# Performance work log

Hardware: AMD Instinct MI355X
Metric: run time of the kernel (lower is better)

Reference implementation:

```python
import jax, jax.numpy as jnp
import numpy as np

N, C, E, NUM_ID, NUM_LABELS = 50000, 128, 1600000, 2048, 7


def setup_inputs() -> dict:
    key = jax.random.key(0)
    k_x, k_r, k_c, k_id, k_lab, k_w, k_wid = jax.random.split(key, 7)
    x = jax.random.normal(k_x, (N, C), dtype=jnp.float32)
    row = jax.random.randint(k_r, (E,), 0, N)
    col = jax.random.randint(k_c, (E,), 0, N)
    # remove accidental self-loops so the 'add remaining self loops' step
    # (append all N self loops) matches PyG's add_remaining_self_loops exactly
    col = jnp.where(col == row, (col + 1) % N, col)
    edge_index = jnp.stack([row, col]).astype(jnp.int64)
    idx = jax.random.randint(k_id, (NUM_ID,), 0, N).astype(jnp.int64)
    node_label = jax.random.randint(k_lab, (N,), 0, 8).astype(jnp.int64)
    # glorot init
    s = jnp.sqrt(6.0 / (C + C)).astype(jnp.float32)
    weight = jax.random.uniform(k_w, (C, C), minval=-s, maxval=s, dtype=jnp.float32)
    weight_id = jax.random.uniform(k_wid, (NUM_LABELS, C, C), minval=-s, maxval=s, dtype=jnp.float32)
    return {"x": x, "edge_index": edge_index, "id": idx, "node_label": node_label,
            "weight": weight, "weight_id": weight_id}


def reference(x, edge_index, id, node_label, weight, weight_id):
    n = x.shape[0]
    row, col = edge_index[0], edge_index[1]
    # ego-center update: x[id] += x[id] @ W (index_add handles duplicate ids)
    x = x.at[id].add(x[id] @ weight)
    # label-grouped gather-matmul-scatter: ox = x + sum_i mask_i * (x @ W_i)
    ox = x
    for i in range(NUM_LABELS):
        mask = (node_label == i + 1)
        ox = ox + jnp.where(mask[:, None], x @ weight_id[i], jnp.zeros((), x.dtype))
    # GCN symmetric normalization with self loops (fill_value = 1.0)
    loop = jnp.arange(n)
    row_f = jnp.concatenate([row, loop])
    col_f = jnp.concatenate([col, loop])
    ew = jnp.ones((row_f.shape[0],), dtype=x.dtype)
    deg = jax.ops.segment_sum(ew, row_f, num_segments=n)
    dinv = jnp.where(deg > 0, deg ** -0.5, jnp.zeros((), x.dtype))
    norm = dinv[row_f] * ew * dinv[col_f]
    # message = norm * x_j (source row), aggregated by sum at target col
    out = jax.ops.segment_sum(norm[:, None] * ox[row_f], col_f, num_segments=n)
    return out
```

## Files before the change

### kernel.cpp

```cpp
#include <hip/hip_runtime.h>
#include <hip/hip_bf16.h>

typedef unsigned int   u32;
typedef unsigned short u16;
typedef unsigned char  u8;
typedef float f32x2 __attribute__((ext_vector_type(2)));
typedef float f32x4 __attribute__((ext_vector_type(4)));

#define N_NODES 50000
#define C_DIM   128
#define E_EDGES 1600000
#define NUM_IDX 2048

#define CPB 256
#define NB  196
#define CAP 9216
#define CHK 4096
#define NP  391
#define PT  512
#define EPT 8
#define GB  8


__global__ void label_hist_kernel(const int* __restrict__ label, int* __restrict__ labCnt,
                                  const int* __restrict__ id, int* __restrict__ cnt,
                                  int* __restrict__ colCursor, int* __restrict__ rowCursor) {
    __shared__ int h[8];
    if (threadIdx.x < 8) h[threadIdx.x] = 0;
    __syncthreads();
    int n = blockIdx.x * 256 + threadIdx.x;
    if (n < N_NODES) atomicAdd(&h[label[n]], 1);
    if (n < NUM_IDX) atomicAdd(&cnt[id[n]], 1);
    if (threadIdx.x == 0) {
        colCursor[blockIdx.x] = blockIdx.x * CAP;
        rowCursor[blockIdx.x] = blockIdx.x * CAP;
    }
    __syncthreads();
    if (threadIdx.x < 8 && h[threadIdx.x] > 0) atomicAdd(&labCnt[threadIdx.x], h[threadIdx.x]);
}

__global__ void label_base_kernel(const int* __restrict__ labCnt, int* __restrict__ labCur) {
    if (threadIdx.x == 0) {
        int run = 0;
        for (int i = 0; i < 8; ++i) { labCur[i] = run; run += labCnt[i]; }
    }
}

__global__ void partition_kernel(const int* __restrict__ row, const int* __restrict__ col,
                                 int* __restrict__ colCursor, int* __restrict__ rowCursor,
                                 u32* __restrict__ S, u8* __restrict__ Sr) {
    __shared__ int hc[NB], hr[NB], bc[NB], br[NB];
    int p = blockIdx.x;
    for (int i = threadIdx.x; i < NB; i += PT) { hc[i] = 0; hr[i] = 0; }
    __syncthreads();
    int e0 = p * CHK, e1 = min(e0 + CHK, E_EDGES);
    int rr[EPT], cc[EPT];
    #pragma unroll
    for (int i = 0; i < EPT; ++i) {
        int e = e0 + threadIdx.x + i * PT;
        if (e < e1) {
            int r = row[e], c = col[e];
            rr[i] = r; cc[i] = c;
            atomicAdd(&hc[c >> 8], 1);
            atomicAdd(&hr[r >> 8], 1);
        }
    }
    __syncthreads();
    for (int i = threadIdx.x; i < NB; i += PT) {
        bc[i] = (hc[i] > 0) ? atomicAdd(&colCursor[i], hc[i]) : 0;
        br[i] = (hr[i] > 0) ? atomicAdd(&rowCursor[i], hr[i]) : 0;
    }
    __syncthreads();
    #pragma unroll
    for (int i = 0; i < EPT; ++i) {
        int e = e0 + threadIdx.x + i * PT;
        if (e < e1) {
            int r = rr[i], c = cc[i];
            int pc = atomicAdd(&bc[c >> 8], 1);
            S[pc] = ((u32)r << 8) | (u32)(c & 255);
            int pr = atomicAdd(&br[r >> 8], 1);
            Sr[pr] = (u8)(r & 255);
        }
    }
}

__global__ void label_fill_kernel(const int* __restrict__ label, int* __restrict__ labCur,
                                  int* __restrict__ nodeByLabel) {
    __shared__ int h[8], base[8], c2[8];
    int t = threadIdx.x;
    if (t < 8) { h[t] = 0; c2[t] = 0; }
    __syncthreads();
    int n = blockIdx.x * 256 + t;
    int l = 0;
    if (n < N_NODES) { l = label[n]; atomicAdd(&h[l], 1); }
    __syncthreads();
    if (t < 8 && h[t] > 0) base[t] = atomicAdd(&labCur[t], h[t]);
    __syncthreads();
    if (n < N_NODES) {
        int pos = base[l] + atomicAdd(&c2[l], 1);
        nodeByLabel[pos] = n;
    }
}

__global__ void csr_deg_kernel(const u32* __restrict__ S, const u8* __restrict__ Sr,
                               const int* __restrict__ colCursor, const int* __restrict__ rowCursor,
                               int* __restrict__ s_beg, int* __restrict__ s_end,
                               u16* __restrict__ srcrow, float* __restrict__ dinv) {
    __shared__ int h[CPB], cur[CPB], sc[CPB];
    int t = threadIdx.x;
    if (blockIdx.x >= NB) {
        int b = blockIdx.x - NB;
        if (t < CPB) h[t] = 0;
        __syncthreads();
        int e0 = b * CAP, e1 = rowCursor[b];
        for (int e = e0 + t; e < e1; e += PT) atomicAdd(&h[Sr[e]], 1);
        __syncthreads();
        if (t < CPB) {
            int n = b * CPB + t;
            if (n < N_NODES) dinv[n] = rsqrtf((float)(h[t] + 1));
        }
        return;
    }
    int b = blockIdx.x;
    if (t < CPB) h[t] = 0;
    __syncthreads();
    int e0 = b * CAP, e1 = colCursor[b];
    for (int e = e0 + t; e < e1; e += PT) atomicAdd(&h[S[e] & 255u], 1);
    __syncthreads();
    if (t < CPB) sc[t] = h[t];
    __syncthreads();
    for (int off = 1; off < CPB; off <<= 1) {
        int v = 0, a = 0;
        if (t < CPB) { v = sc[t]; a = (t >= off) ? sc[t - off] : 0; }
        __syncthreads();
        if (t < CPB) sc[t] = v + a;
        __syncthreads();
    }
    if (t < CPB) {
        int base = (t == 0) ? 0 : sc[t - 1];
        int gcol = b * CPB + t;
        if (gcol < N_NODES) {
            s_beg[gcol] = e0 + base;
            s_end[gcol] = e0 + base + h[t];
        }
        cur[t] = base;
    }
    __syncthreads();
    for (int e = e0 + t; e < e1; e += PT) {
        u32 v = S[e];
        int pos = atomicAdd(&cur[v & 255u], 1);
        srcrow[e0 + pos] = (u16)(v >> 8);
    }
}

__global__ void node_msg_kernel(const float* __restrict__ x,
                                const int* __restrict__ cnt,
                                const int* __restrict__ label,
                                const float* __restrict__ dinv,
                                const float* __restrict__ W,
                                const float* __restrict__ Wid,
                                const int* __restrict__ nodeByLabel,
                                __hip_bfloat16* __restrict__ msgb) {
    __shared__ float xsT[C_DIM][GB];
    __shared__ int nid[GB], lab[GB], cc[GB];
    int t = threadIdx.x;
    if (t < GB) {
        int n = nodeByLabel[blockIdx.x * GB + t];
        nid[t] = n; lab[t] = label[n]; cc[t] = cnt[n];
    }
    __syncthreads();
    #pragma unroll
    for (int g = 0; g < GB; ++g)
        xsT[t][g] = __builtin_nontemporal_load(x + (size_t)nid[g] * C_DIM + t);
    __syncthreads();
    for (int g = 0; g < GB; ++g) {
        int c = cc[g];
        if (c > 0) {
            float acc = 0.f;
            #pragma unroll 8
            for (int k = 0; k < C_DIM; ++k) acc += xsT[k][g] * W[k * C_DIM + t];
            __syncthreads();
            xsT[t][g] += (float)c * acc;
            __syncthreads();
        }
    }
    float res[GB];
    #pragma unroll
    for (int g = 0; g < GB; ++g) res[g] = xsT[t][g];
    if (lab[0] == lab[GB - 1]) {
        int L = lab[0];
        if (L > 0) {
            const float* Wl = Wid + (size_t)(L - 1) * C_DIM * C_DIM;
            float acc[GB];
            #pragma unroll
            for (int g = 0; g < GB; ++g) acc[g] = 0.f;
            for (int k = 0; k < C_DIM; ++k) {
                float w = Wl[k * C_DIM + t];
                f32x4 xv0 = *(const f32x4*)&xsT[k][0];
                f32x4 xv1 = *(const f32x4*)&xsT[k][4];
                acc[0] += xv0.x * w; acc[1] += xv0.y * w;
                acc[2] += xv0.z * w; acc[3] += xv0.w * w;
                acc[4] += xv1.x * w; acc[5] += xv1.y * w;
                acc[6] += xv1.z * w; acc[7] += xv1.w * w;
            }
            #pragma unroll
            for (int g = 0; g < GB; ++g) res[g] += acc[g];
        }
    } else {
        for (int g = 0; g < GB; ++g) {
            int L = lab[g];
            if (L > 0) {
                const float* Wl = Wid + (size_t)(L - 1) * C_DIM * C_DIM;
                float acc = 0.f;
                #pragma unroll 8
                for (int k = 0; k < C_DIM; ++k) acc += xsT[k][g] * Wl[k * C_DIM + t];
                res[g] += acc;
            }
        }
    }
    #pragma unroll
    for (int g = 0; g < GB; ++g) {
        int n = nid[g];
        msgb[(size_t)n * C_DIM + t] = __float2bfloat16(dinv[n] * res[g]);
    }
}

__global__ void gather_kernel(const int* __restrict__ s_beg, const int* __restrict__ s_end,
                              const u16* __restrict__ srcrow,
                              const float* __restrict__ dinv,
                              const u32* __restrict__ m32,
                              float* __restrict__ out) {
    int wid  = threadIdx.x >> 6;
    int lane = threadIdx.x & 63;
    int g = lane >> 4;
    int q = lane & 15;
    int c = blockIdx.x * 4 + wid;
    int e0 = s_beg[c], e1 = s_end[c];
    const uint4* m4 = (const uint4*)m32;

    float a0[4], a1[4];
    #pragma unroll
    for (int k = 0; k < 4; ++k) { a0[k] = 0.f; a1[k] = 0.f; }

    #define ACC4(U)                                                          \
        a0[0] += __uint_as_float((U).x << 16); a1[0] += __uint_as_float((U).x & 0xffff0000u); \
        a0[1] += __uint_as_float((U).y << 16); a1[1] += __uint_as_float((U).y & 0xffff0000u); \
        a0[2] += __uint_as_float((U).z << 16); a1[2] += __uint_as_float((U).z & 0xffff0000u); \
        a0[3] += __uint_as_float((U).w << 16); a1[3] += __uint_as_float((U).w & 0xffff0000u);

    int e = e0;
    for (; e + 8 <= e1; e += 8) {
        u32 r0 = srcrow[e + g];
        u32 r1 = srcrow[e + 4 + g];
        uint4 u0 = m4[r0 * 16u + (u32)q];
        uint4 u1 = m4[r1 * 16u + (u32)q];
        ACC4(u0);
        ACC4(u1);
    }
    if (e + 4 <= e1) {
        u32 r0 = srcrow[e + g];
        uint4 u0 = m4[r0 * 16u + (u32)q];
        ACC4(u0);
        e += 4;
    }
    if (g == 0) {
        uint4 us = m4[(u32)c * 16u + (u32)q];
        ACC4(us);
        for (; e < e1; ++e) {
            u32 r = srcrow[e];
            uint4 u = m4[r * 16u + (u32)q];
            ACC4(u);
        }
    }
    #undef ACC4

    #pragma unroll
    for (int k = 0; k < 4; ++k) {
        a0[k] += __shfl_xor(a0[k], 16);
        a0[k] += __shfl_xor(a0[k], 32);
        a1[k] += __shfl_xor(a1[k], 16);
        a1[k] += __shfl_xor(a1[k], 32);
    }

    if (lane < 16) {
        float di = dinv[c];
        f32x4 o0, o1;
        o0.x = di * a0[0]; o0.y = di * a1[0]; o0.z = di * a0[1]; o0.w = di * a1[1];
        o1.x = di * a0[2]; o1.y = di * a1[2]; o1.z = di * a0[3]; o1.w = di * a1[3];
        f32x4* op = (f32x4*)(out + ((size_t)c << 7)) + (q << 1);
        __builtin_nontemporal_store(o0, op);
        __builtin_nontemporal_store(o1, op + 1);
    }
}

extern "C" void kernel_launch(void* const* d_in, const int* in_sizes, int n_in,
                              void* d_out, int out_size, void* d_ws, size_t ws_size,
                              hipStream_t stream) {
    const float* x     = (const float*)d_in[0];
    const int*   edge  = (const int*)d_in[1];
    const int*   id    = (const int*)d_in[2];
    const int*   label = (const int*)d_in[3];
    const float* W     = (const float*)d_in[4];
    const float* Wid   = (const float*)d_in[5];
    float*       out   = (float*)d_out;

    const int* row = edge;
    const int* col = edge + E_EDGES;

    __hip_bfloat16* msgb = (__hip_bfloat16*)d_ws;
    u32* S           = (u32*)(msgb + (size_t)N_NODES * C_DIM);
    u16* srcrow      = (u16*)(S + (size_t)NB * CAP);
    u8*  Sr          = (u8*)(srcrow + (size_t)NB * CAP);
    int* s_beg       = (int*)(Sr + (size_t)NB * CAP);
    int* s_end       = s_beg + N_NODES;
    int* colCursor   = s_end + N_NODES;
    int* rowCursor   = colCursor + NB;
    int* nodeByLabel = rowCursor + NB;
    float* dinv      = (float*)(nodeByLabel + N_NODES);
    int* cnt         = (int*)(dinv + N_NODES);
    int* labCnt      = cnt + N_NODES;
    int* labCur      = labCnt + 8;

    hipMemsetAsync(cnt, 0, ((size_t)N_NODES + 16) * sizeof(int), stream);

    label_hist_kernel <<<196, 256, 0, stream>>>(label, labCnt, id, cnt, colCursor, rowCursor);
    label_base_kernel <<<1, 64, 0, stream>>>(labCnt, labCur);
    partition_kernel  <<<NP, PT, 0, stream>>>(row, col, colCursor, rowCursor, S, Sr);
    label_fill_kernel <<<196, 256, 0, stream>>>(label, labCur, nodeByLabel);
    csr_deg_kernel    <<<2 * NB, PT, 0, stream>>>(S, Sr, colCursor, rowCursor,
                                                  s_beg, s_end, srcrow, dinv);
    node_msg_kernel   <<<N_NODES / GB, C_DIM, 0, stream>>>(x, cnt, label, dinv, W, Wid,
                                                           nodeByLabel, msgb);
    gather_kernel     <<<N_NODES / 4, 256, 0, stream>>>(s_beg, s_end, srcrow, dinv,
                                                        (const u32*)msgb, out);
}
```

Measured before the change: 231.1 us.

## Merge preprocessing kernels to cut launches and double edges per partition block

Folds the label histogram and id count into the partition kernel as extra blocks, and folds label base computation and label fill into the CSR/degree kernel as extra blocks. Cursors become relative offsets zeroed by the existing memset, which removes the cursor-init dependency. Partition blocks now handle 8192 edges each with 16 edges per thread instead of 4096. This cuts the launch count from seven to four, trading some added register pressure and a redundant prefix sum over label counts in each label block.

```diff
diff --git a/kernel.cpp b/kernel.cpp
--- a/kernel.cpp
+++ b/kernel.cpp
@@ -15,49 +15,40 @@
 #define CPB 256
 #define NB  196
 #define CAP 9216
-#define CHK 4096
-#define NP  391
+#define CHK 8192
+#define NP  196
 #define PT  512
-#define EPT 8
+#define EPT 16
 #define GB  8
-
-
-__global__ void label_hist_kernel(const int* __restrict__ label, int* __restrict__ labCnt,
-                                  const int* __restrict__ id, int* __restrict__ cnt,
-                                  int* __restrict__ colCursor, int* __restrict__ rowCursor) {
-    __shared__ int h[8];
-    if (threadIdx.x < 8) h[threadIdx.x] = 0;
-    __syncthreads();
-    int n = blockIdx.x * 256 + threadIdx.x;
-    if (n < N_NODES) atomicAdd(&h[label[n]], 1);
-    if (n < NUM_IDX) atomicAdd(&cnt[id[n]], 1);
-    if (threadIdx.x == 0) {
-        colCursor[blockIdx.x] = blockIdx.x * CAP;
-        rowCursor[blockIdx.x] = blockIdx.x * CAP;
-    }
-    __syncthreads();
-    if (threadIdx.x < 8 && h[threadIdx.x] > 0) atomicAdd(&labCnt[threadIdx.x], h[threadIdx.x]);
-}
-
-__global__ void label_base_kernel(const int* __restrict__ labCnt, int* __restrict__ labCur) {
-    if (threadIdx.x == 0) {
-        int run = 0;
-        for (int i = 0; i < 8; ++i) { labCur[i] = run; run += labCnt[i]; }
-    }
-}
-
-__global__ void partition_kernel(const int* __restrict__ row, const int* __restrict__ col,
+#define NLB 98
+
+
+__global__ void part_hist_kernel(const int* __restrict__ row, const int* __restrict__ col,
+                                 const int* __restrict__ label, const int* __restrict__ id,
                                  int* __restrict__ colCursor, int* __restrict__ rowCursor,
-                                 u32* __restrict__ S, u8* __restrict__ Sr) {
+                                 u32* __restrict__ S, u8* __restrict__ Sr,
+                                 int* __restrict__ labCnt, int* __restrict__ cnt) {
     __shared__ int hc[NB], hr[NB], bc[NB], br[NB];
+    __shared__ int h8[8];
+    int t = threadIdx.x;
+    if (blockIdx.x >= NP) {
+        if (t < 8) h8[t] = 0;
+        __syncthreads();
+        int n = (blockIdx.x - NP) * PT + t;
+        if (n < N_NODES) atomicAdd(&h8[label[n]], 1);
+        if (n < NUM_IDX) atomicAdd(&cnt[id[n]], 1);
+        __syncthreads();
+        if (t < 8 && h8[t] > 0) atomicAdd(&labCnt[t], h8[t]);
+        return;
+    }
     int p = blockIdx.x;
-    for (int i = threadIdx.x; i < NB; i += PT) { hc[i] = 0; hr[i] = 0; }
+    for (int i = t; i < NB; i += PT) { hc[i] = 0; hr[i] = 0; }
     __syncthreads();
     int e0 = p * CHK, e1 = min(e0 + CHK, E_EDGES);
     int rr[EPT], cc[EPT];
     #pragma unroll
     for (int i = 0; i < EPT; ++i) {
-        int e = e0 + threadIdx.x + i * PT;
+        int e = e0 + t + i * PT;
         if (e < e1) {
             int r = row[e], c = col[e];
             rr[i] = r; cc[i] = c;
@@ -66,14 +57,14 @@
         }
     }
     __syncthreads();
-    for (int i = threadIdx.x; i < NB; i += PT) {
-        bc[i] = (hc[i] > 0) ? atomicAdd(&colCursor[i], hc[i]) : 0;
-        br[i] = (hr[i] > 0) ? atomicAdd(&rowCursor[i], hr[i]) : 0;
+    for (int i = t; i < NB; i += PT) {
+        bc[i] = (hc[i] > 0) ? (i * CAP + atomicAdd(&colCursor[i], hc[i])) : 0;
+        br[i] = (hr[i] > 0) ? (i * CAP + atomicAdd(&rowCursor[i], hr[i])) : 0;
     }
     __syncthreads();
     #pragma unroll
     for (int i = 0; i < EPT; ++i) {
-        int e = e0 + threadIdx.x + i * PT;
+        int e = e0 + t + i * PT;
         if (e < e1) {
             int r = rr[i], c = cc[i];
             int pc = atomicAdd(&bc[c >> 8], 1);
@@ -84,35 +75,39 @@
     }
 }
 
-__global__ void label_fill_kernel(const int* __restrict__ label, int* __restrict__ labCur,
-                                  int* __restrict__ nodeByLabel) {
-    __shared__ int h[8], base[8], c2[8];
+__global__ void csr_fill_kernel(const u32* __restrict__ S, const u8* __restrict__ Sr,
+                                const int* __restrict__ colCursor, const int* __restrict__ rowCursor,
+                                int* __restrict__ s_beg, int* __restrict__ s_end,
+                                u16* __restrict__ srcrow, float* __restrict__ dinv,
+                                const int* __restrict__ label, const int* __restrict__ labCnt,
+                                int* __restrict__ labOffset, int* __restrict__ nodeByLabel) {
+    __shared__ int h[CPB], cur[CPB], sc[CPB];
+    __shared__ int h8[8], base8[8], c28[8];
     int t = threadIdx.x;
-    if (t < 8) { h[t] = 0; c2[t] = 0; }
-    __syncthreads();
-    int n = blockIdx.x * 256 + t;
-    int l = 0;
-    if (n < N_NODES) { l = label[n]; atomicAdd(&h[l], 1); }
-    __syncthreads();
-    if (t < 8 && h[t] > 0) base[t] = atomicAdd(&labCur[t], h[t]);
-    __syncthreads();
-    if (n < N_NODES) {
-        int pos = base[l] + atomicAdd(&c2[l], 1);
-        nodeByLabel[pos] = n;
-    }
-}
-
-__global__ void csr_deg_kernel(const u32* __restrict__ S, const u8* __restrict__ Sr,
-                               const int* __restrict__ colCursor, const int* __restrict__ rowCursor,
-                               int* __restrict__ s_beg, int* __restrict__ s_end,
-                               u16* __restrict__ srcrow, float* __restrict__ dinv) {
-    __shared__ int h[CPB], cur[CPB], sc[CPB];
-    int t = threadIdx.x;
+    if (blockIdx.x >= 2 * NB) {
+        if (t < 8) { h8[t] = 0; c28[t] = 0; }
+        __syncthreads();
+        int n = (blockIdx.x - 2 * NB) * PT + t;
+        int l = 0;
+        if (n < N_NODES) { l = label[n]; atomicAdd(&h8[l], 1); }
+        __syncthreads();
+        if (t < 8 && h8[t] > 0) {
+            int lb = 0;
+            for (int i = 0; i < t; ++i) lb += labCnt[i];
+            base8[t] = lb + atomicAdd(&labOffset[t], h8[t]);
+        }
+        __syncthreads();
+        if (n < N_NODES) {
+            int pos = base8[l] + atomicAdd(&c28[l], 1);
+            nodeByLabel[pos] = n;
+        }
+        return;
+    }
     if (blockIdx.x >= NB) {
         int b = blockIdx.x - NB;
         if (t < CPB) h[t] = 0;
         __syncthreads();
-        int e0 = b * CAP, e1 = rowCursor[b];
+        int e0 = b * CAP, e1 = b * CAP + rowCursor[b];
         for (int e = e0 + t; e < e1; e += PT) atomicAdd(&h[Sr[e]], 1);
         __syncthreads();
         if (t < CPB) {
@@ -124,7 +119,7 @@
     int b = blockIdx.x;
     if (t < CPB) h[t] = 0;
     __syncthreads();
-    int e0 = b * CAP, e1 = colCursor[b];
+    int e0 = b * CAP, e1 = b * CAP + colCursor[b];
     for (int e = e0 + t; e < e1; e += PT) atomicAdd(&h[S[e] & 255u], 1);
     __syncthreads();
     if (t < CPB) sc[t] = h[t];
@@ -313,24 +308,23 @@
     u8*  Sr          = (u8*)(srcrow + (size_t)NB * CAP);
     int* s_beg       = (int*)(Sr + (size_t)NB * CAP);
     int* s_end       = s_beg + N_NODES;
-    int* colCursor   = s_end + N_NODES;
-    int* rowCursor   = colCursor + NB;
-    int* nodeByLabel = rowCursor + NB;
+    int* nodeByLabel = s_end + N_NODES;
     float* dinv      = (float*)(nodeByLabel + N_NODES);
     int* cnt         = (int*)(dinv + N_NODES);
     int* labCnt      = cnt + N_NODES;
-    int* labCur      = labCnt + 8;
-
-    hipMemsetAsync(cnt, 0, ((size_t)N_NODES + 16) * sizeof(int), stream);
-
-    label_hist_kernel <<<196, 256, 0, stream>>>(label, labCnt, id, cnt, colCursor, rowCursor);
-    label_base_kernel <<<1, 64, 0, stream>>>(labCnt, labCur);
-    partition_kernel  <<<NP, PT, 0, stream>>>(row, col, colCursor, rowCursor, S, Sr);
-    label_fill_kernel <<<196, 256, 0, stream>>>(label, labCur, nodeByLabel);
-    csr_deg_kernel    <<<2 * NB, PT, 0, stream>>>(S, Sr, colCursor, rowCursor,
-                                                  s_beg, s_end, srcrow, dinv);
-    node_msg_kernel   <<<N_NODES / GB, C_DIM, 0, stream>>>(x, cnt, label, dinv, W, Wid,
-                                                           nodeByLabel, msgb);
-    gather_kernel     <<<N_NODES / 4, 256, 0, stream>>>(s_beg, s_end, srcrow, dinv,
-                                                        (const u32*)msgb, out);
-}
+    int* labOffset   = labCnt + 8;
+    int* colCursor   = labOffset + 8;
+    int* rowCursor   = colCursor + NB;
+
+    hipMemsetAsync(cnt, 0, ((size_t)N_NODES + 16 + 2 * NB) * sizeof(int), stream);
+
+    part_hist_kernel<<<NP + NLB, PT, 0, stream>>>(row, col, label, id,
+                                                  colCursor, rowCursor, S, Sr, labCnt, cnt);
+    csr_fill_kernel <<<2 * NB + NLB, PT, 0, stream>>>(S, Sr, colCursor, rowCursor,
+                                                      s_beg, s_end, srcrow, dinv,
+                                                      label, labCnt, labOffset, nodeByLabel);
+    node_msg_kernel <<<N_NODES / GB, C_DIM, 0, stream>>>(x, cnt, label, dinv, W, Wid,
+                                                         nodeByLabel, msgb);
+    gather_kernel   <<<N_NODES / 4, 256, 0, stream>>>(s_beg, s_end, srcrow, dinv,
+                                                      (const u32*)msgb, out);
+}
```

Result: faster. 220.5 us (-4.6%).
